# Kernel optimization log

Measured on AMD Instinct MI355X. Metric: run time of the kernel, lower is better.

## Reference

```python
import jax, jax.numpy as jnp
import numpy as np

N_EMBED = 1024
N_HEAD = 16
HEAD_DIM = N_EMBED // N_HEAD


def setup_inputs() -> dict:
    key = jax.random.key(0)
    k1, k2, k3, k4, k5 = jax.random.split(key, 5)
    x = jax.random.normal(k1, (4, 2048, N_EMBED), dtype=jnp.float32)
    s = 1.0 / np.sqrt(N_EMBED)
    W_attn = jax.random.normal(k2, (N_EMBED, 3 * N_EMBED), dtype=jnp.float32) * s
    b_attn = jnp.zeros((3 * N_EMBED,), dtype=jnp.float32)
    W_proj = jax.random.normal(k3, (N_EMBED, N_EMBED), dtype=jnp.float32) * s
    b_proj = jnp.zeros((N_EMBED,), dtype=jnp.float32)
    return {"x": x, "W_attn": W_attn, "b_attn": b_attn, "W_proj": W_proj, "b_proj": b_proj}


def reference(x, W_attn, b_attn, W_proj, b_proj):
    B, T, C = x.shape
    qkv = x @ W_attn + b_attn  # [B, T, 3C]
    q, k, v = jnp.split(qkv, 3, axis=2)
    # [B, H, T, D]
    q = q.reshape(B, T, N_HEAD, HEAD_DIM).transpose(0, 2, 1, 3)
    k = k.reshape(B, T, N_HEAD, HEAD_DIM).transpose(0, 2, 1, 3)
    v = v.reshape(B, T, N_HEAD, HEAD_DIM).transpose(0, 2, 1, 3)
    scale = 1.0 / np.sqrt(HEAD_DIM)
    scores = jnp.einsum('bhqd,bhkd->bhqk', q, k) * scale
    causal = jnp.tril(jnp.ones((T, T), dtype=bool))
    scores = jnp.where(causal[None, None], scores, -jnp.inf)
    attn = jax.nn.softmax(scores, axis=-1)
    y = jnp.einsum('bhqk,bhkd->bhqd', attn, v)
    y = y.transpose(0, 2, 1, 3).reshape(B, T, C)
    return y @ W_proj + b_proj
```

## Files before the change

kernel.cpp:

```cpp
#include <hip/hip_runtime.h>

typedef unsigned short u16;
typedef unsigned int u32;
typedef unsigned long long u64;
typedef __attribute__((ext_vector_type(8))) __bf16 b8;
typedef __attribute__((ext_vector_type(4))) float f32x4;

#define T_SEQ 2048
#define NB 4
#define NH 16
#define HD 64
#define CEMB 1024
#define M_ROWS (NB * T_SEQ)
#define Q_PRESCALE 0.18033688011112042f

__device__ __forceinline__ u16 f2bf(float f) {
  union { float f; unsigned int u; } v; v.f = f;
  unsigned int r = v.u + 0x7FFFu + ((v.u >> 16) & 1u);
  return (u16)(r >> 16);
}

__device__ __forceinline__ u32 pk2bf(float a, float b) {
  __bf16 x = (__bf16)a, y = (__bf16)b;
  return (u32)*(u16*)&x | ((u32)*(u16*)&y << 16);
}

__device__ __forceinline__ void gl_lds16(const u16* g, u16* l) {
  __builtin_amdgcn_global_load_lds(
      (const __attribute__((address_space(1))) unsigned int*)g,
      (__attribute__((address_space(3))) unsigned int*)l, 16, 0, 0);
}

#define BARRIER() __builtin_amdgcn_s_barrier()
#define LGKM0() do { asm volatile("s_waitcnt lgkmcnt(0)" ::: "memory"); \
                     __builtin_amdgcn_sched_barrier(0); } while (0)
#define VMCNT4() asm volatile("s_waitcnt vmcnt(4)" ::: "memory")
#define VMCNT2() asm volatile("s_waitcnt vmcnt(2)" ::: "memory")
#define VMCNT0() asm volatile("s_waitcnt vmcnt(0)" ::: "memory")

__global__ void k_convert(const float* __restrict__ in, u16* __restrict__ out, int n4) {
  int i = blockIdx.x * blockDim.x + threadIdx.x;
  int stride = gridDim.x * blockDim.x;
  for (; i < n4; i += stride) {
    float4 v = ((const float4*)in)[i];
    ushort4 o;
    o.x = f2bf(v.x); o.y = f2bf(v.y); o.z = f2bf(v.z); o.w = f2bf(v.w);
    ((ushort4*)out)[i] = o;
  }
}

__global__ __launch_bounds__(256) void k_transpose(const float* __restrict__ W,
                                                   u16* __restrict__ Wt, int K, int N) {
  __shared__ u16 t[64][65];
  int k0 = blockIdx.y * 64, n0 = blockIdx.x * 64;
  int tx = threadIdx.x & 63, ty = threadIdx.x >> 6;
  for (int i = ty; i < 64; i += 4)
    t[i][tx] = f2bf(W[(size_t)(k0 + i) * N + n0 + tx]);
  __syncthreads();
  for (int i = ty; i < 64; i += 4)
    Wt[(size_t)(n0 + i) * K + k0 + tx] = t[tx][i];
}

template <int MODE, int BNU>
__global__ __launch_bounds__(512, 2) void k_gemm8(const u16* __restrict__ A,
                                                  const u16* __restrict__ Bt,
                                                  const float* __restrict__ bias,
                                                  u16* __restrict__ out_bf,
                                                  float* __restrict__ out_f,
                                                  u16* __restrict__ vt,
                                                  int M, int N, int K, int mstripe) {
  __shared__ u16 sA[2][16384];
  __shared__ u16 sB[2][BNU * 4096];
  constexpr int NI = BNU / 2;
  const int tid = threadIdx.x;
  const int lane = tid & 63;
  const int wid = tid >> 6;
  const int wm = wid >> 2;
  const int wn = wid & 3;
  const int fr = lane & 15;
  const int g = lane >> 4;

  const int xcd = blockIdx.x & 7;
  const int idx = blockIdx.x >> 3;
  const int mt = xcd * mstripe + (idx % mstripe);
  const int nt = idx / mstripe;
  const int row0 = mt * 256, col0 = nt * (BNU * 64);
  const int NT = K >> 6;

  const int kswz = ((lane & 7) ^ ((lane >> 3) & 7)) * 8;
  const u16* gA = A + (size_t)(row0 + wid * 8 + (lane >> 3)) * K + kswz;
  const u16* gB = Bt + (size_t)(col0 + wid * 8 + (lane >> 3)) * K + kswz;

#define SGA(buf, T, u) gl_lds16(gA + (size_t)(u) * 64 * K + (size_t)(T) * 64, \
                                &sA[buf][(u) * 4096 + wid * 512])
#define SGB(buf, T, u) gl_lds16(gB + (size_t)(u) * 64 * K + (size_t)(T) * 64, \
                                &sB[buf][(u) * 4096 + wid * 512])
#define RDA(dst, rowe, ks)                                                     \
  { int row_ = (rowe);                                                         \
    dst = *(const b8*)&sA[bufc][row_ * 64 + ((((ks)*4 + g) ^ (row_ & 7)) << 3)]; }
#define RDB(dst, cole, ks)                                                     \
  { int col_ = (cole);                                                         \
    dst = *(const b8*)&sB[bufc][col_ * 64 + ((((ks)*4 + g) ^ (col_ & 7)) << 3)]; }

  f32x4 acc[8][BNU] = {};
  b8 aF[4][2], bF0[NI][2], bF1[NI][2];

#pragma unroll
  for (int u = 0; u < BNU; ++u) SGB(0, 0, u);
  SGA(0, 0, 0); SGA(0, 0, 2);
  SGA(0, 0, 1); SGA(0, 0, 3);
  SGA(1, 1, 0); SGA(1, 1, 2);
  VMCNT4();
  BARRIER();
  __builtin_amdgcn_sched_barrier(0);

#pragma unroll 2
  for (int T = 0; T < NT; ++T) {
    const int bufc = T & 1, bufn = bufc ^ 1;
    const bool st1 = (T + 1 < NT), st2 = (T + 2 < NT);

#pragma unroll
    for (int mi = 0; mi < 4; ++mi)
#pragma unroll
      for (int ks = 0; ks < 2; ++ks) RDA(aF[mi][ks], wm * 128 + mi * 16 + fr, ks);
#pragma unroll
    for (int ni = 0; ni < NI; ++ni)
#pragma unroll
      for (int ks = 0; ks < 2; ++ks) RDB(bF0[ni][ks], wn * (BNU * 16) + ni * 16 + fr, ks);
    if (st1) { SGB(bufn, T + 1, 0); SGB(bufn, T + 1, 1); }
    else VMCNT0();
    BARRIER(); LGKM0();
    __builtin_amdgcn_s_setprio(1);
#pragma unroll
    for (int mi = 0; mi < 4; ++mi)
#pragma unroll
      for (int ni = 0; ni < NI; ++ni)
#pragma unroll
        for (int ks = 0; ks < 2; ++ks)
          acc[mi][ni] = __builtin_amdgcn_mfma_f32_16x16x32_bf16(aF[mi][ks], bF0[ni][ks], acc[mi][ni], 0, 0, 0);
    __builtin_amdgcn_s_setprio(0);
    __builtin_amdgcn_sched_barrier(0);
    BARRIER();

#pragma unroll
    for (int ni = 0; ni < NI; ++ni)
#pragma unroll
      for (int ks = 0; ks < 2; ++ks) RDB(bF1[ni][ks], wn * (BNU * 16) + (NI + ni) * 16 + fr, ks);
    if (BNU == 4 && st1) { SGB(bufn, T + 1, 2); SGB(bufn, T + 1, 3); }
    if constexpr (BNU == 4) { VMCNT4(); } else { VMCNT2(); }
    BARRIER(); LGKM0();
    __builtin_amdgcn_s_setprio(1);
#pragma unroll
    for (int mi = 0; mi < 4; ++mi)
#pragma unroll
      for (int ni = 0; ni < NI; ++ni)
#pragma unroll
        for (int ks = 0; ks < 2; ++ks)
          acc[mi][NI + ni] = __builtin_amdgcn_mfma_f32_16x16x32_bf16(aF[mi][ks], bF1[ni][ks], acc[mi][NI + ni], 0, 0, 0);
    __builtin_amdgcn_s_setprio(0);
    __builtin_amdgcn_sched_barrier(0);
    BARRIER();

#pragma unroll
    for (int mi = 0; mi < 4; ++mi)
#pragma unroll
      for (int ks = 0; ks < 2; ++ks) RDA(aF[mi][ks], wm * 128 + 64 + mi * 16 + fr, ks);
    if (st2) { SGA(bufc, T + 2, 0); SGA(bufc, T + 2, 2); }
    BARRIER(); LGKM0();
    __builtin_amdgcn_s_setprio(1);
#pragma unroll
    for (int mi = 0; mi < 4; ++mi)
#pragma unroll
      for (int ni = 0; ni < NI; ++ni)
#pragma unroll
        for (int ks = 0; ks < 2; ++ks)
          acc[4 + mi][ni] = __builtin_amdgcn_mfma_f32_16x16x32_bf16(aF[mi][ks], bF0[ni][ks], acc[4 + mi][ni], 0, 0, 0);
    __builtin_amdgcn_s_setprio(0);
    __builtin_amdgcn_sched_barrier(0);
    BARRIER();

    if (st1) { SGA(bufn, T + 1, 1); SGA(bufn, T + 1, 3); }
    VMCNT4();
    BARRIER();
    __builtin_amdgcn_sched_barrier(0);
    __builtin_amdgcn_s_setprio(1);
#pragma unroll
    for (int mi = 0; mi < 4; ++mi)
#pragma unroll
      for (int ni = 0; ni < NI; ++ni)
#pragma unroll
        for (int ks = 0; ks < 2; ++ks)
          acc[4 + mi][NI + ni] = __builtin_amdgcn_mfma_f32_16x16x32_bf16(aF[mi][ks], bF1[ni][ks], acc[4 + mi][NI + ni], 0, 0, 0);
    __builtin_amdgcn_s_setprio(0);
    __builtin_amdgcn_sched_barrier(0);
    BARRIER();
  }
#undef SGA
#undef SGB
#undef RDA
#undef RDB

  const int fg = lane >> 4;
  if (MODE != 2) {
#pragma unroll
    for (int ni = 0; ni < BNU; ++ni) {
      int col = col0 + wn * (BNU * 16) + ni * 16 + fr;
      float bv = bias[col];
#pragma unroll
      for (int mi = 0; mi < 8; ++mi) {
#pragma unroll
        for (int r = 0; r < 4; ++r) {
          int row = row0 + wm * 128 + mi * 16 + fg * 4 + r;
          float v = acc[mi][ni][r] + bv;
          if (MODE == 0) {
            float sc = (col < CEMB) ? Q_PRESCALE : 1.0f;
            out_bf[(size_t)row * (2 * CEMB) + col] = f2bf(v * sc);
          } else {
            out_f[(size_t)row * N + col] = v;
          }
        }
      }
    }
  } else {
    u16* st = (u16*)sA;
    const int bq = row0 >> 11;
    const int t0g = row0 & (T_SEQ - 1);
#pragma unroll
    for (int pass = 0; pass < 2; ++pass) {
      __syncthreads();
      if ((wn >> 1) == pass) {
#pragma unroll
        for (int nn = 0; nn < BNU; ++nn) {
          const int hdl = (wn & 1) * 32 + nn * 16 + fr;
          const float bv = bias[col0 + pass * 64 + hdl];
#pragma unroll
          for (int mi = 0; mi < 8; ++mi) {
            const int tl = wm * 128 + mi * 16 + fg * 4;
#pragma unroll
            for (int rp = 0; rp < 2; ++rp) {
              u32 pk = pk2bf(acc[mi][nn][2 * rp] + bv, acc[mi][nn][2 * rp + 1] + bv);
              *(u32*)&st[hdl * 280 + tl + 2 * rp] = pk;
            }
          }
        }
      }
      __syncthreads();
      const int hd_r = tid >> 3;
      const int ck = tid & 7;
      u16* vrow = vt + ((size_t)(bq * (NH * HD) + col0 + pass * 64 + hd_r)) * T_SEQ + t0g;
#pragma unroll
      for (int j = 0; j < 4; ++j) {
        const int chunk = ck + 8 * j;
        f32x4 d = *(const f32x4*)&st[hd_r * 280 + chunk * 8];
        *(f32x4*)&vrow[chunk * 8] = d;
      }
    }
  }
}

__global__ __launch_bounds__(256, 4) void k_attn(const u16* __restrict__ qk,
                                                 const u16* __restrict__ vtg,
                                                 u16* __restrict__ y) {
  __shared__ __align__(16) u16 kt_s[2][64 * 64];
  __shared__ __align__(16) u16 vt_s[2][64 * 64];
  __shared__ __align__(16) char pl_s[4][2048];

  const int lane = threadIdx.x & 63;
  const int wave = threadIdx.x >> 6;
  const int tid = threadIdx.x;
  const int g = lane >> 4, c = lane & 15;

  const int xcd = blockIdx.x & 7;
  const int idx = blockIdx.x >> 3;
  const int bh = xcd * 8 + (idx & 7);
  const int pr = idx >> 3;
  const int b = bh >> 4, h = bh & 15;

  char* plw = pl_s[wave];
  char* plA = plw + c * 128;
  const int b3 = c >> 3;
  const int e2 = (c & 7) << 1;
  const int sb = g + b3 * 8;

  b8 ones_frag;
#pragma unroll
  for (int e = 0; e < 8; ++e) ones_frag[e] = (c == 0) ? (__bf16)1.0f : (__bf16)0.0f;

  const int srow = tid >> 3;
  const int scc = (tid & 7) ^ (srow & 7);
  const u16* ksrc0 = qk + ((size_t)(b * T_SEQ) + srow) * (2 * CEMB) + CEMB + h * HD + scc * 8;
  const u16* vsrc0 = vtg + ((size_t)(bh * HD) + srow) * T_SEQ + scc * 8;

#define STAGE(t, bb)                                                    \
  {                                                                     \
    const u16* ks_ = ksrc0 + (size_t)(t) * 64 * (2 * CEMB);             \
    const u16* vs_ = vsrc0 + (t) * 64;                                  \
    gl_lds16(ks_, &kt_s[bb][wave * 512]);                               \
    gl_lds16(ks_ + 32 * (2 * CEMB), &kt_s[bb][wave * 512 + 2048]);      \
    gl_lds16(vs_, &vt_s[bb][wave * 512]);                               \
    gl_lds16(vs_ + 32 * T_SEQ, &vt_s[bb][wave * 512 + 2048]);           \
  }

#pragma unroll 1
  for (int seg = 0; seg < 2; ++seg) {
    const int tt = seg ? pr : (31 - pr);
    const int qW = tt * 64 + wave * 16;

    const u16* qrow = qk + (size_t)(b * T_SEQ + qW + c) * (2 * CEMB) + h * HD + g * 8;
    const b8 qf0 = *(const b8*)qrow;
    const b8 qf1 = *(const b8*)(qrow + 32);

    float m = -3e38f;
    f32x4 o[4] = {};
    f32x4 o4 = {0.f, 0.f, 0.f, 0.f};

    const int ntt = tt + 1;
    int cur = 0;
    STAGE(0, 0);
    __syncthreads();

    for (int t = 0; t < ntt; ++t) {
      if (t + 1 < ntt) STAGE(t + 1, cur ^ 1);
      const int k0 = t * 64;
      const bool diag = (t == ntt - 1);
      const u16* kt = kt_s[cur];
      const u16* vtl = vt_s[cur];

      f32x4 s[4] = {{0.f,0.f,0.f,0.f},{0.f,0.f,0.f,0.f},{0.f,0.f,0.f,0.f},{0.f,0.f,0.f,0.f}};
      __builtin_amdgcn_s_setprio(1);
#pragma unroll
      for (int n = 0; n < 4; ++n) {
        if (!diag || n <= wave) {
          const b8 kf0 = *(const b8*)&kt[(n * 16 + c) * 64 + ((g ^ (c & 7)) << 3)];
          const b8 kf1 = *(const b8*)&kt[(n * 16 + c) * 64 + (((4 + g) ^ (c & 7)) << 3)];
          s[n] = __builtin_amdgcn_mfma_f32_16x16x32_bf16(kf0, qf0, s[n], 0, 0, 0);
          s[n] = __builtin_amdgcn_mfma_f32_16x16x32_bf16(kf1, qf1, s[n], 0, 0, 0);
        }
      }
      __builtin_amdgcn_s_setprio(0);

      if (diag) {
#pragma unroll
        for (int n = 0; n < 4; ++n)
#pragma unroll
          for (int r = 0; r < 4; ++r)
            if (k0 + n * 16 + g * 4 + r > qW + c) s[n][r] = -3e38f;
      }

      float rm = fmaxf(fmaxf(fmaxf(s[0][0], s[0][1]), s[0][2]),
                       fmaxf(fmaxf(s[0][3], s[1][0]), s[1][1]));
      rm = fmaxf(rm, fmaxf(fmaxf(s[1][2], s[1][3]), s[2][0]));
      rm = fmaxf(rm, fmaxf(fmaxf(s[2][1], s[2][2]), s[2][3]));
      rm = fmaxf(rm, fmaxf(fmaxf(s[3][0], s[3][1]), fmaxf(s[3][2], s[3][3])));
      rm = fmaxf(rm, __shfl_xor(rm, 16));
      rm = fmaxf(rm, __shfl_xor(rm, 32));

      if (!__all(rm <= m + 8.0f)) {
        float mn = fmaxf(m, rm);
        float al = __builtin_amdgcn_exp2f(m - mn);
        m = mn;
#pragma unroll
        for (int r = 0; r < 4; ++r) {
          int src = (lane & 48) + g * 4 + r;
          float a = __shfl(al, src);
#pragma unroll
          for (int nt = 0; nt < 4; ++nt) o[nt][r] *= a;
          o4[r] *= a;
        }
      }

#pragma unroll
      for (int n = 0; n < 4; ++n) {
        u32 lo = pk2bf(__builtin_amdgcn_exp2f(s[n][0] - m),
                       __builtin_amdgcn_exp2f(s[n][1] - m));
        u32 hi = pk2bf(__builtin_amdgcn_exp2f(s[n][2] - m),
                       __builtin_amdgcn_exp2f(s[n][3] - m));
        *(u64*)(plA + ((((4 * n + sb) & 15) ^ e2) << 3)) = ((u64)hi << 32) | lo;
      }

      b8 vb[2][4];
#pragma unroll
      for (int ks = 0; ks < 2; ++ks)
#pragma unroll
        for (int nt = 0; nt < 4; ++nt)
          vb[ks][nt] = *(const b8*)&vtl[(nt * 16 + c) * 64 + (((ks * 4 + g) ^ (c & 7)) << 3)];

      asm volatile("s_waitcnt lgkmcnt(0)" ::: "memory");
      __builtin_amdgcn_sched_barrier(0);

      __builtin_amdgcn_s_setprio(1);
#pragma unroll
      for (int ks = 0; ks < 2; ++ks) {
        const b8 pa = *(const b8*)(plA + ((((ks * 8 + 2 * g + 8 * b3) & 15) ^ e2) << 3));
        o4 = __builtin_amdgcn_mfma_f32_16x16x32_bf16(pa, ones_frag, o4, 0, 0, 0);
#pragma unroll
        for (int nt = 0; nt < 4; ++nt)
          o[nt] = __builtin_amdgcn_mfma_f32_16x16x32_bf16(pa, vb[ks][nt], o[nt], 0, 0, 0);
      }
      __builtin_amdgcn_s_setprio(0);

      __syncthreads();
      cur ^= 1;
    }

#pragma unroll
    for (int r = 0; r < 4; ++r) {
      float lr = __shfl(o4[r], lane & 48);
      float inv = 1.0f / lr;
#pragma unroll
      for (int nt = 0; nt < 4; ++nt) {
        __bf16 ov = (__bf16)(o[nt][r] * inv);
        y[(size_t)(b * T_SEQ + qW + g * 4 + r) * CEMB + h * HD + nt * 16 + c] = *(u16*)&ov;
      }
    }
  }
#undef STAGE
}

extern "C" void kernel_launch(void* const* d_in, const int* in_sizes, int n_in,
                              void* d_out, int out_size, void* d_ws, size_t ws_size,
                              hipStream_t stream) {
  const float* x = (const float*)d_in[0];
  const float* W_attn = (const float*)d_in[1];
  const float* b_attn = (const float*)d_in[2];
  const float* W_proj = (const float*)d_in[3];
  const float* b_proj = (const float*)d_in[4];
  float* out = (float*)d_out;

  char* ws = (char*)d_ws;
  u16* x_bf    = (u16*)(ws);
  u16* wattn_t = (u16*)(ws + 16777216);
  u16* wproj_t = (u16*)(ws + 23068672);
  u16* qk_bf   = (u16*)(ws + 25165824);
  u16* vt      = (u16*)(ws + 58720256);
  u16* y_bf    = (u16*)(ws + 75497472);

  k_convert<<<2048, 256, 0, stream>>>(x, x_bf, (NB * T_SEQ * CEMB) / 4);
  k_transpose<<<dim3(3 * CEMB / 64, CEMB / 64), 256, 0, stream>>>(W_attn, wattn_t, CEMB, 3 * CEMB);
  k_transpose<<<dim3(CEMB / 64, CEMB / 64), 256, 0, stream>>>(W_proj, wproj_t, CEMB, CEMB);
  k_gemm8<0, 4><<<256, 512, 0, stream>>>(x_bf, wattn_t, b_attn, qk_bf, nullptr, nullptr,
                                         M_ROWS, 2 * CEMB, CEMB, 4);
  k_gemm8<2, 2><<<256, 512, 0, stream>>>(x_bf, wattn_t + 2048 * CEMB, b_attn + 2 * CEMB,
                                         nullptr, nullptr, vt, M_ROWS, CEMB, CEMB, 4);
  k_attn<<<1024, 256, 0, stream>>>(qk_bf, vt, y_bf);
  k_gemm8<1, 2><<<256, 512, 0, stream>>>(y_bf, wproj_t, b_proj, nullptr, out, nullptr,
                                         M_ROWS, CEMB, CEMB, 4);
}
```

Before: 184.4 us.

## Load K and V fragments directly from global memory, dropping LDS staging

```diff
diff --git a/kernel.cpp b/kernel.cpp
--- a/kernel.cpp
+++ b/kernel.cpp
@@ -258,16 +258,13 @@
   }
 }
 
-__global__ __launch_bounds__(256, 4) void k_attn(const u16* __restrict__ qk,
+__global__ __launch_bounds__(256, 6) void k_attn(const u16* __restrict__ qk,
                                                  const u16* __restrict__ vtg,
                                                  u16* __restrict__ y) {
-  __shared__ __align__(16) u16 kt_s[2][64 * 64];
-  __shared__ __align__(16) u16 vt_s[2][64 * 64];
   __shared__ __align__(16) char pl_s[4][2048];
 
   const int lane = threadIdx.x & 63;
   const int wave = threadIdx.x >> 6;
-  const int tid = threadIdx.x;
   const int g = lane >> 4, c = lane & 15;
 
   const int xcd = blockIdx.x & 7;
@@ -276,8 +273,7 @@
   const int pr = idx >> 3;
   const int b = bh >> 4, h = bh & 15;
 
-  char* plw = pl_s[wave];
-  char* plA = plw + c * 128;
+  char* plA = pl_s[wave] + c * 128;
   const int b3 = c >> 3;
   const int e2 = (c & 7) << 1;
   const int sb = g + b3 * 8;
@@ -286,20 +282,8 @@
 #pragma unroll
   for (int e = 0; e < 8; ++e) ones_frag[e] = (c == 0) ? (__bf16)1.0f : (__bf16)0.0f;
 
-  const int srow = tid >> 3;
-  const int scc = (tid & 7) ^ (srow & 7);
-  const u16* ksrc0 = qk + ((size_t)(b * T_SEQ) + srow) * (2 * CEMB) + CEMB + h * HD + scc * 8;
-  const u16* vsrc0 = vtg + ((size_t)(bh * HD) + srow) * T_SEQ + scc * 8;
-
-#define STAGE(t, bb)                                                    \
-  {                                                                     \
-    const u16* ks_ = ksrc0 + (size_t)(t) * 64 * (2 * CEMB);             \
-    const u16* vs_ = vsrc0 + (t) * 64;                                  \
-    gl_lds16(ks_, &kt_s[bb][wave * 512]);                               \
-    gl_lds16(ks_ + 32 * (2 * CEMB), &kt_s[bb][wave * 512 + 2048]);      \
-    gl_lds16(vs_, &vt_s[bb][wave * 512]);                               \
-    gl_lds16(vs_ + 32 * T_SEQ, &vt_s[bb][wave * 512 + 2048]);           \
-  }
+  const u16* kbase = qk + (size_t)(b * T_SEQ) * (2 * CEMB) + CEMB + h * HD;
+  const u16* vbase = vtg + (size_t)(bh * HD) * T_SEQ;
 
 #pragma unroll 1
   for (int seg = 0; seg < 2; ++seg) {
@@ -315,26 +299,34 @@
     f32x4 o4 = {0.f, 0.f, 0.f, 0.f};
 
     const int ntt = tt + 1;
-    int cur = 0;
-    STAGE(0, 0);
-    __syncthreads();
 
     for (int t = 0; t < ntt; ++t) {
-      if (t + 1 < ntt) STAGE(t + 1, cur ^ 1);
       const int k0 = t * 64;
       const bool diag = (t == ntt - 1);
-      const u16* kt = kt_s[cur];
-      const u16* vtl = vt_s[cur];
+
+      b8 kf0[4], kf1[4];
+#pragma unroll
+      for (int n = 0; n < 4; ++n) {
+        if (!diag || n <= wave) {
+          const u16* kr = kbase + (size_t)(k0 + n * 16 + c) * (2 * CEMB) + g * 8;
+          kf0[n] = *(const b8*)kr;
+          kf1[n] = *(const b8*)(kr + 32);
+        }
+      }
+      b8 vb[2][4];
+#pragma unroll
+      for (int ks = 0; ks < 2; ++ks)
+#pragma unroll
+        for (int nt = 0; nt < 4; ++nt)
+          vb[ks][nt] = *(const b8*)&vbase[(size_t)(nt * 16 + c) * T_SEQ + k0 + ks * 32 + g * 8];
 
       f32x4 s[4] = {{0.f,0.f,0.f,0.f},{0.f,0.f,0.f,0.f},{0.f,0.f,0.f,0.f},{0.f,0.f,0.f,0.f}};
       __builtin_amdgcn_s_setprio(1);
 #pragma unroll
       for (int n = 0; n < 4; ++n) {
         if (!diag || n <= wave) {
-          const b8 kf0 = *(const b8*)&kt[(n * 16 + c) * 64 + ((g ^ (c & 7)) << 3)];
-          const b8 kf1 = *(const b8*)&kt[(n * 16 + c) * 64 + (((4 + g) ^ (c & 7)) << 3)];
-          s[n] = __builtin_amdgcn_mfma_f32_16x16x32_bf16(kf0, qf0, s[n], 0, 0, 0);
-          s[n] = __builtin_amdgcn_mfma_f32_16x16x32_bf16(kf1, qf1, s[n], 0, 0, 0);
+          s[n] = __builtin_amdgcn_mfma_f32_16x16x32_bf16(kf0[n], qf0, s[n], 0, 0, 0);
+          s[n] = __builtin_amdgcn_mfma_f32_16x16x32_bf16(kf1[n], qf1, s[n], 0, 0, 0);
         }
       }
       __builtin_amdgcn_s_setprio(0);
@@ -378,16 +370,6 @@
         *(u64*)(plA + ((((4 * n + sb) & 15) ^ e2) << 3)) = ((u64)hi << 32) | lo;
       }
 
-      b8 vb[2][4];
-#pragma unroll
-      for (int ks = 0; ks < 2; ++ks)
-#pragma unroll
-        for (int nt = 0; nt < 4; ++nt)
-          vb[ks][nt] = *(const b8*)&vtl[(nt * 16 + c) * 64 + (((ks * 4 + g) ^ (c & 7)) << 3)];
-
-      asm volatile("s_waitcnt lgkmcnt(0)" ::: "memory");
-      __builtin_amdgcn_sched_barrier(0);
-
       __builtin_amdgcn_s_setprio(1);
 #pragma unroll
       for (int ks = 0; ks < 2; ++ks) {
@@ -398,9 +380,6 @@
           o[nt] = __builtin_amdgcn_mfma_f32_16x16x32_bf16(pa, vb[ks][nt], o[nt], 0, 0, 0);
       }
       __builtin_amdgcn_s_setprio(0);
-
-      __syncthreads();
-      cur ^= 1;
     }
 
 #pragma unroll
@@ -414,7 +393,6 @@
       }
     }
   }
-#undef STAGE
 }
 
 extern "C" void kernel_launch(void* const* d_in, const int* in_sizes, int n_in,
```

New measurement: 671.1 us. 3.64x slower.
